# Kernel tuning notes

Hardware: AMD Instinct MI355X
Metric: run time of the kernel (lower is better)

Reference implementation:

```python
import jax, jax.numpy as jnp
import numpy as np

N_NODES = 100000
N_EDGES = 1600000
F_IN = 32
F_OUT = 32


def setup_inputs() -> dict:
    key = jax.random.key(0)
    k_x, k_r, k_c, k_v, k_w, k_b = jax.random.split(key, 6)
    x = jax.random.normal(k_x, (N_NODES, F_IN), dtype=jnp.float32)
    edge_rows = jnp.sort(jax.random.randint(k_r, (N_EDGES,), 0, N_NODES, dtype=jnp.int32))
    edge_cols = jax.random.randint(k_c, (N_EDGES,), 0, N_NODES, dtype=jnp.int32)
    edge_vals = jax.random.uniform(k_v, (N_EDGES,), dtype=jnp.float32)
    # nn.Linear params: weight [out, in], bias [out]
    bound = 1.0 / np.sqrt(F_IN)
    W = jax.random.uniform(k_w, (F_OUT, F_IN), minval=-bound, maxval=bound, dtype=jnp.float32)
    b = jax.random.uniform(k_b, (F_OUT,), minval=-bound, maxval=bound, dtype=jnp.float32)
    return {"x": x, "edge_rows": edge_rows, "edge_cols": edge_cols,
            "edge_vals": edge_vals, "W": W, "b": b}


def reference(x, edge_rows, edge_cols, edge_vals, W, b):
    # adj @ x  (COO spmm): gather source features, scale by edge weight,
    # scatter-add into destination rows.
    msgs = x[edge_cols] * edge_vals[:, None]                 # [E, F_in]
    agg = jax.ops.segment_sum(msgs, edge_rows,
                              num_segments=x.shape[0],
                              indices_are_sorted=True)       # [N, F_in]
    # linear + relu: agg @ W.T + b
    return jax.nn.relu(agg @ W.T + b)                        # [N, F_out]
```

## Files before the change

### kernel.cpp

```cpp
#include <hip/hip_runtime.h>

#define F 32

typedef __attribute__((ext_vector_type(8))) unsigned short us8;
typedef __attribute__((ext_vector_type(4))) float f4;

static __device__ __forceinline__ unsigned short f2bf(float f) {
    unsigned int u = __float_as_uint(f);
    u += 0x7FFF + ((u >> 16) & 1);
    return (unsigned short)(u >> 16);
}
static __device__ __forceinline__ float bf2f(unsigned short s) {
    return __uint_as_float(((unsigned int)s) << 16);
}

__global__ __launch_bounds__(256) void prologue_kernel(
    const float* __restrict__ x, const float* __restrict__ W,
    const int* __restrict__ rows,
    unsigned short* __restrict__ y, int* __restrict__ ptr,
    int N, int E, int nxw) {
    int b = blockIdx.x;
    int t = threadIdx.x;
    if (b < nxw) {
        __shared__ float Wt[F * F];
        __shared__ float xs[64 * F];
        #pragma unroll
        for (int k = 0; k < 4; ++k) {
            int i = t + k * 256;
            Wt[(i & 31) * F + (i >> 5)] = W[i];
        }
        int n0 = b * 64;
        const f4* __restrict__ x4 = (const f4*)(x + (size_t)n0 * F);
        f4* __restrict__ xs4 = (f4*)xs;
        int limit4 = (N * F - n0 * F) >> 2;
        #pragma unroll
        for (int k = 0; k < 2; ++k) {
            int i = t + k * 256;
            f4 z = {0.f, 0.f, 0.f, 0.f};
            xs4[i] = (i < limit4) ? x4[i] : z;
        }
        __syncthreads();
        int fo = t & 31;
        int j0 = (t >> 5) * 8;
        #pragma unroll
        for (int j = 0; j < 8; ++j) {
            int nl = j0 + j;
            float acc = 0.0f;
            #pragma unroll
            for (int fi = 0; fi < F; ++fi)
                acc = fmaf(xs[nl * F + fi], Wt[fi * F + fo], acc);
            int n = n0 + nl;
            if (n < N) y[(size_t)n * F + fo] = f2bf(acc);
        }
    } else {
        int e = (b - nxw) * 256 + t;
        if (e > E) return;
        int prev = (e == 0) ? -1 : rows[e - 1];
        int cur  = (e == E) ? N  : rows[e];
        for (int r = prev + 1; r <= cur; ++r) ptr[r] = e;
    }
}

__global__ __launch_bounds__(256) void gnn_kernel(
    const unsigned short* __restrict__ y,
    const int*   __restrict__ cols,
    const float* __restrict__ vals,
    const int*   __restrict__ row_ptr,
    const float* __restrict__ bias,
    float*       __restrict__ out, int N) {
    int t = threadIdx.x;
    int lane = t & 63;
    int g = lane >> 2;
    int l = lane & 3;
    int n = (blockIdx.x * 4 + (t >> 6)) * 16 + g;
    int start = 0, end = 0;
    if (n < N) { start = row_ptr[n]; end = row_ptr[n + 1]; }

    const us8* __restrict__ y8 = (const us8*)y;

    float a0[8], a1[8];
    #pragma unroll
    for (int i = 0; i < 8; ++i) { a0[i] = 0.f; a1[i] = 0.f; }

    for (int e = start; e < end; e += 8) {
        int ec[8];
        #pragma unroll
        for (int k = 0; k < 8; ++k) {
            int ek = e + k;
            ec[k] = (ek < end) ? ek : (end - 1);
        }
        int c[8];
        #pragma unroll
        for (int k = 0; k < 8; ++k) c[k] = cols[ec[k]];
        float v[8];
        #pragma unroll
        for (int k = 0; k < 8; ++k) {
            float vv = vals[ec[k]];
            v[k] = (e + k < end) ? vv : 0.0f;
        }
        us8 r[8];
        #pragma unroll
        for (int k = 0; k < 8; ++k) r[k] = y8[(size_t)c[k] * 4 + l];
        #pragma unroll
        for (int k = 0; k < 8; ++k) {
            float* a = (k & 1) ? a1 : a0;
            #pragma unroll
            for (int i = 0; i < 8; ++i)
                a[i] = fmaf(bf2f(r[k][i]), v[k], a[i]);
        }
    }

    if (n < N) {
        const float* __restrict__ bp = bias + l * 8;
        f4 o0, o1;
        o0.x = fmaxf(a0[0] + a1[0] + bp[0], 0.f);
        o0.y = fmaxf(a0[1] + a1[1] + bp[1], 0.f);
        o0.z = fmaxf(a0[2] + a1[2] + bp[2], 0.f);
        o0.w = fmaxf(a0[3] + a1[3] + bp[3], 0.f);
        o1.x = fmaxf(a0[4] + a1[4] + bp[4], 0.f);
        o1.y = fmaxf(a0[5] + a1[5] + bp[5], 0.f);
        o1.z = fmaxf(a0[6] + a1[6] + bp[6], 0.f);
        o1.w = fmaxf(a0[7] + a1[7] + bp[7], 0.f);
        f4* op = (f4*)(out + (size_t)n * F + l * 8);
        __builtin_nontemporal_store(o0, op);
        __builtin_nontemporal_store(o1, op + 1);
    }
}

__global__ __launch_bounds__(256) void gnn_fp32_kernel(
    const float* __restrict__ x,
    const int*   __restrict__ rows,
    const int*   __restrict__ cols,
    const float* __restrict__ vals,
    const float* __restrict__ W,
    const float* __restrict__ bias,
    float*       __restrict__ out,
    int N, int E) {
    __shared__ float Wt[F * F];
    __shared__ float bS[F];
    int t = threadIdx.x;
    for (int i = t; i < F * F; i += 256)
        Wt[(i & 31) * F + (i >> 5)] = W[i];
    if (t < F) bS[t] = bias[t];
    __syncthreads();
    int lane = t & 63;
    int n = blockIdx.x * 4 + (t >> 6);
    if (n >= N) return;
    int g = lane >> 3, l = lane & 7;
    int target = n + (lane >> 5);
    int lo = 0, hi = E;
    while (lo < hi) { int mid = (lo + hi) >> 1; if (rows[mid] < target) lo = mid + 1; else hi = mid; }
    int start = __shfl(lo, 0), end = __shfl(lo, 32);
    const float4* __restrict__ x4 = (const float4*)x;
    float4 acc0 = {0,0,0,0}, acc1 = {0,0,0,0};
    for (int e0 = start; e0 < end; e0 += 16) {
        int ea = e0 + g, eb = ea + 8;
        if (ea < end) { int c = cols[ea]; float v = vals[ea]; float4 xr = x4[c * 8 + l];
            acc0.x = fmaf(xr.x, v, acc0.x); acc0.y = fmaf(xr.y, v, acc0.y);
            acc0.z = fmaf(xr.z, v, acc0.z); acc0.w = fmaf(xr.w, v, acc0.w); }
        if (eb < end) { int c = cols[eb]; float v = vals[eb]; float4 xr = x4[c * 8 + l];
            acc1.x = fmaf(xr.x, v, acc1.x); acc1.y = fmaf(xr.y, v, acc1.y);
            acc1.z = fmaf(xr.z, v, acc1.z); acc1.w = fmaf(xr.w, v, acc1.w); }
    }
    acc0.x += acc1.x; acc0.y += acc1.y; acc0.z += acc1.z; acc0.w += acc1.w;
    #pragma unroll
    for (int m = 8; m < 64; m <<= 1) {
        acc0.x += __shfl_xor(acc0.x, m); acc0.y += __shfl_xor(acc0.y, m);
        acc0.z += __shfl_xor(acc0.z, m); acc0.w += __shfl_xor(acc0.w, m);
    }
    float comp[4] = {acc0.x, acc0.y, acc0.z, acc0.w};
    int fo = lane & 31;
    float o = bS[fo];
    #pragma unroll
    for (int fi = 0; fi < F; ++fi)
        o = fmaf(__shfl(comp[fi & 3], fi >> 2), Wt[fi * F + fo], o);
    if (lane < F) out[n * F + fo] = fmaxf(o, 0.0f);
}

extern "C" void kernel_launch(void* const* d_in, const int* in_sizes, int n_in,
                              void* d_out, int out_size, void* d_ws, size_t ws_size,
                              hipStream_t stream) {
    const float* x    = (const float*)d_in[0];
    const int*   rows = (const int*)  d_in[1];
    const int*   cols = (const int*)  d_in[2];
    const float* vals = (const float*)d_in[3];
    const float* W    = (const float*)d_in[4];
    const float* bias = (const float*)d_in[5];
    float*       out  = (float*)d_out;

    int N = in_sizes[0] / F;
    int E = in_sizes[1];

    size_t rp_bytes = (size_t)(N + 1) * sizeof(int);
    size_t y_off    = (rp_bytes + 255) & ~(size_t)255;
    size_t need     = y_off + (size_t)N * F * sizeof(unsigned short);

    if (ws_size >= need) {
        int* row_ptr = (int*)d_ws;
        unsigned short* y = (unsigned short*)((char*)d_ws + y_off);
        int nxw  = (N + 63) / 64;
        int ncsr = (E + 1 + 255) / 256;
        prologue_kernel<<<nxw + ncsr, 256, 0, stream>>>(x, W, rows, y, row_ptr, N, E, nxw);
        gnn_kernel<<<(N + 63) / 64, 256, 0, stream>>>(y, cols, vals, row_ptr, bias, out, N);
    } else {
        gnn_fp32_kernel<<<(N + 3) / 4, 256, 0, stream>>>(
            x, rows, cols, vals, W, bias, out, N, E);
    }
}
```

Before: 113.1 us.

## Use split-bf16 MFMA for x@W.T prologue and software-pipeline edge gather

```diff
diff --git a/kernel.cpp b/kernel.cpp
--- a/kernel.cpp
+++ b/kernel.cpp
@@ -3,7 +3,9 @@
 #define F 32
 
 typedef __attribute__((ext_vector_type(8))) unsigned short us8;
+typedef __attribute__((ext_vector_type(4))) unsigned short us4;
 typedef __attribute__((ext_vector_type(4))) float f4;
+typedef __attribute__((ext_vector_type(8))) __bf16 bf8;
 
 static __device__ __forceinline__ unsigned short f2bf(float f) {
     unsigned int u = __float_as_uint(f);
@@ -22,35 +24,57 @@
     int b = blockIdx.x;
     int t = threadIdx.x;
     if (b < nxw) {
-        __shared__ float Wt[F * F];
-        __shared__ float xs[64 * F];
-        #pragma unroll
-        for (int k = 0; k < 4; ++k) {
-            int i = t + k * 256;
-            Wt[(i & 31) * F + (i >> 5)] = W[i];
-        }
-        int n0 = b * 64;
-        const f4* __restrict__ x4 = (const f4*)(x + (size_t)n0 * F);
-        f4* __restrict__ xs4 = (f4*)xs;
-        int limit4 = (N * F - n0 * F) >> 2;
-        #pragma unroll
-        for (int k = 0; k < 2; ++k) {
-            int i = t + k * 256;
-            f4 z = {0.f, 0.f, 0.f, 0.f};
-            xs4[i] = (i < limit4) ? x4[i] : z;
-        }
-        __syncthreads();
-        int fo = t & 31;
-        int j0 = (t >> 5) * 8;
-        #pragma unroll
-        for (int j = 0; j < 8; ++j) {
-            int nl = j0 + j;
-            float acc = 0.0f;
-            #pragma unroll
-            for (int fi = 0; fi < F; ++fi)
-                acc = fmaf(xs[nl * F + fi], Wt[fi * F + fo], acc);
-            int n = n0 + nl;
-            if (n < N) y[(size_t)n * F + fo] = f2bf(acc);
+        int lane = t & 63;
+        int n0 = (b * 4 + (t >> 6)) * 16;
+        if (n0 >= N) return;
+        int m  = lane & 15;
+        int kb = lane >> 4;
+        int k0 = kb * 8;
+
+        int ra = n0 + m; if (ra > N - 1) ra = N - 1;
+        const f4* __restrict__ xr = (const f4*)(x + (size_t)ra * F + k0);
+        f4 xa = xr[0], xb = xr[1];
+        float fx[8] = {xa.x, xa.y, xa.z, xa.w, xb.x, xb.y, xb.z, xb.w};
+        bf8 Ah, Al;
+        #pragma unroll
+        for (int i = 0; i < 8; ++i) {
+            __bf16 h = (__bf16)fx[i];
+            Ah[i] = h;
+            Al[i] = (__bf16)(fx[i] - (float)h);
+        }
+
+        const f4* __restrict__ w0 = (const f4*)(W + (size_t)m * F + k0);
+        const f4* __restrict__ w1 = (const f4*)(W + (size_t)(m + 16) * F + k0);
+        f4 wa = w0[0], wb = w0[1], wc = w1[0], wd = w1[1];
+        float fw0[8] = {wa.x, wa.y, wa.z, wa.w, wb.x, wb.y, wb.z, wb.w};
+        float fw1[8] = {wc.x, wc.y, wc.z, wc.w, wd.x, wd.y, wd.z, wd.w};
+        bf8 B0h, B0l, B1h, B1l;
+        #pragma unroll
+        for (int i = 0; i < 8; ++i) {
+            __bf16 h0 = (__bf16)fw0[i];
+            B0h[i] = h0;
+            B0l[i] = (__bf16)(fw0[i] - (float)h0);
+            __bf16 h1 = (__bf16)fw1[i];
+            B1h[i] = h1;
+            B1l[i] = (__bf16)(fw1[i] - (float)h1);
+        }
+
+        f4 acc0 = {0.f, 0.f, 0.f, 0.f}, acc1 = {0.f, 0.f, 0.f, 0.f};
+        acc0 = __builtin_amdgcn_mfma_f32_16x16x32_bf16(Ah, B0h, acc0, 0, 0, 0);
+        acc0 = __builtin_amdgcn_mfma_f32_16x16x32_bf16(Ah, B0l, acc0, 0, 0, 0);
+        acc0 = __builtin_amdgcn_mfma_f32_16x16x32_bf16(Al, B0h, acc0, 0, 0, 0);
+        acc1 = __builtin_amdgcn_mfma_f32_16x16x32_bf16(Ah, B1h, acc1, 0, 0, 0);
+        acc1 = __builtin_amdgcn_mfma_f32_16x16x32_bf16(Ah, B1l, acc1, 0, 0, 0);
+        acc1 = __builtin_amdgcn_mfma_f32_16x16x32_bf16(Al, B1h, acc1, 0, 0, 0);
+
+        int mr = n0 + kb * 4;
+        #pragma unroll
+        for (int r = 0; r < 4; ++r) {
+            int row = mr + r;
+            if (row < N) {
+                y[(size_t)row * F + m]      = f2bf(acc0[r]);
+                y[(size_t)row * F + m + 16] = f2bf(acc1[r]);
+            }
         }
     } else {
         int e = (b - nxw) * 256 + t;
@@ -70,60 +94,65 @@
     float*       __restrict__ out, int N) {
     int t = threadIdx.x;
     int lane = t & 63;
-    int g = lane >> 2;
-    int l = lane & 3;
-    int n = (blockIdx.x * 4 + (t >> 6)) * 16 + g;
+    int g = lane >> 3;
+    int l = lane & 7;
+    int n = (blockIdx.x * 4 + (t >> 6)) * 8 + g;
     int start = 0, end = 0;
     if (n < N) { start = row_ptr[n]; end = row_ptr[n + 1]; }
 
-    const us8* __restrict__ y8 = (const us8*)y;
-
-    float a0[8], a1[8];
-    #pragma unroll
-    for (int i = 0; i < 8; ++i) { a0[i] = 0.f; a1[i] = 0.f; }
+    const us4* __restrict__ y4 = (const us4*)y;
+
+    float a0[4], a1[4];
+    #pragma unroll
+    for (int i = 0; i < 4; ++i) { a0[i] = 0.f; a1[i] = 0.f; }
+
+    int lim = end - 1; if (lim < 0) lim = 0;
+
+    int cc[8]; float vv[8];
+    #pragma unroll
+    for (int k = 0; k < 8; ++k) {
+        int ek = start + k;
+        int ec = (ek < end) ? ek : lim;
+        cc[k] = cols[ec];
+        vv[k] = vals[ec];
+    }
 
     for (int e = start; e < end; e += 8) {
-        int ec[8];
+        int c[8]; float v[8];
         #pragma unroll
         for (int k = 0; k < 8; ++k) {
-            int ek = e + k;
-            ec[k] = (ek < end) ? ek : (end - 1);
-        }
-        int c[8];
-        #pragma unroll
-        for (int k = 0; k < 8; ++k) c[k] = cols[ec[k]];
-        float v[8];
+            c[k] = cc[k];
+            v[k] = (e + k < end) ? vv[k] : 0.0f;
+        }
         #pragma unroll
         for (int k = 0; k < 8; ++k) {
-            float vv = vals[ec[k]];
-            v[k] = (e + k < end) ? vv : 0.0f;
-        }
-        us8 r[8];
-        #pragma unroll
-        for (int k = 0; k < 8; ++k) r[k] = y8[(size_t)c[k] * 4 + l];
+            int ek = e + 8 + k;
+            int ec = (ek < end) ? ek : lim;
+            cc[k] = cols[ec];
+            vv[k] = vals[ec];
+        }
+        us4 r[8];
+        #pragma unroll
+        for (int k = 0; k < 8; ++k) r[k] = y4[(size_t)c[k] * 8 + l];
         #pragma unroll
         for (int k = 0; k < 8; ++k) {
             float* a = (k & 1) ? a1 : a0;
             #pragma unroll
-            for (int i = 0; i < 8; ++i)
+            for (int i = 0; i < 4; ++i)
                 a[i] = fmaf(bf2f(r[k][i]), v[k], a[i]);
         }
     }
 
     if (n < N) {
-        const float* __restrict__ bp = bias + l * 8;
-        f4 o0, o1;
-        o0.x = fmaxf(a0[0] + a1[0] + bp[0], 0.f);
-        o0.y = fmaxf(a0[1] + a1[1] + bp[1], 0.f);
-        o0.z = fmaxf(a0[2] + a1[2] + bp[2], 0.f);
-        o0.w = fmaxf(a0[3] + a1[3] + bp[3], 0.f);
-        o1.x = fmaxf(a0[4] + a1[4] + bp[4], 0.f);
-        o1.y = fmaxf(a0[5] + a1[5] + bp[5], 0.f);
-        o1.z = fmaxf(a0[6] + a1[6] + bp[6], 0.f);
-        o1.w = fmaxf(a0[7] + a1[7] + bp[7], 0.f);
-        f4* op = (f4*)(out + (size_t)n * F + l * 8);
-        __builtin_nontemporal_store(o0, op);
-        __builtin_nontemporal_store(o1, op + 1);
+        const f4* __restrict__ b4 = (const f4*)bias;
+        f4 bb = b4[l];
+        f4 o;
+        o.x = fmaxf(a0[0] + a1[0] + bb.x, 0.f);
+        o.y = fmaxf(a0[1] + a1[1] + bb.y, 0.f);
+        o.z = fmaxf(a0[2] + a1[2] + bb.z, 0.f);
+        o.w = fmaxf(a0[3] + a1[3] + bb.w, 0.f);
+        f4* op = (f4*)(out + (size_t)n * F + l * 4);
+        __builtin_nontemporal_store(o, op);
     }
 }
 
@@ -201,7 +230,7 @@
         int nxw  = (N + 63) / 64;
         int ncsr = (E + 1 + 255) / 256;
         prologue_kernel<<<nxw + ncsr, 256, 0, stream>>>(x, W, rows, y, row_ptr, N, E, nxw);
-        gnn_kernel<<<(N + 63) / 64, 256, 0, stream>>>(y, cols, vals, row_ptr, bias, out, N);
+        gnn_kernel<<<(N + 31) / 32, 256, 0, stream>>>(y, cols, vals, row_ptr, bias, out, N);
     } else {
         gnn_fp32_kernel<<<(N + 3) / 4, 256, 0, stream>>>(
             x, rows, cols, vals, W, bias, out, N, E);
```

Result: no change. 111.7 us, median of 2 (-1.2%).
